# Kernel tuning notes

Hardware: AMD Instinct MI355X
Metric: run time of the kernel (lower is better)

Reference implementation:

```python
import jax, jax.numpy as jnp
import numpy as np
import math

SIZE = 11
PAD = 5
C1 = 0.01 ** 2
C2 = 0.03 ** 2


def gaussian_window():
    # Matches torch __init__: 1D gaussian (sigma=1.5), normalized, outer product,
    # expanded to depthwise weight of shape (3, 1, 11, 11)
    x = np.arange(SIZE, dtype=np.float32)
    g = np.exp(-((x - SIZE // 2) ** 2) / (2.0 * 1.5 ** 2)).astype(np.float32)
    g = g / g.sum()
    w2d = np.outer(g, g).astype(np.float32)  # (11, 11)
    return jnp.asarray(np.broadcast_to(w2d, (3, 1, SIZE, SIZE)).copy())


def depthwise_conv(x, win):
    return jax.lax.conv_general_dilated(
        x, win,
        window_strides=(1, 1),
        padding=[(PAD, PAD), (PAD, PAD)],
        dimension_numbers=('NCHW', 'OIHW', 'NCHW'),
        feature_group_count=3,
    )


def setup_inputs() -> dict:
    key = jax.random.key(0)
    k1, k2 = jax.random.split(key)
    img1 = jax.random.uniform(k1, (16, 3, 512, 512), dtype=jnp.float32)
    img2 = jax.random.uniform(k2, (16, 3, 512, 512), dtype=jnp.float32)
    return {"img1": img1, "img2": img2, "win": gaussian_window()}


def reference(img1, img2, win):
    mu1 = depthwise_conv(img1, win)
    mu2 = depthwise_conv(img2, win)
    mu1_sq = mu1 * mu1
    mu2_sq = mu2 * mu2
    mu1_mu2 = mu1 * mu2
    sig1_sq = depthwise_conv(img1 * img1, win) - mu1_sq
    sig2_sq = depthwise_conv(img2 * img2, win) - mu2_sq
    sig12 = depthwise_conv(img1 * img2, win) - mu1_mu2
    v = ((2.0 * mu1_mu2 + C1) * (2.0 * sig12 + C2)) / (
        (mu1_sq + mu2_sq + C1) * (sig1_sq + sig2_sq + C2))
    return 1.0 - jnp.mean(v)
```

## Files before the change

### kernel.cpp

```cpp
#include <hip/hip_runtime.h>


#define IMG 512
#define NPIX (16LL * 3 * 512 * 512)
#define GX 4
#define GY 16
#define NBLK (GX * GY * 48)
#define NPART (NBLK * 4)
#define HP 56

typedef short v8s __attribute__((ext_vector_type(8)));
typedef float v4f __attribute__((ext_vector_type(4)));
typedef __bf16 bf2 __attribute__((ext_vector_type(2)));
typedef float f2  __attribute__((ext_vector_type(2)));

static __device__ __forceinline__ int cvtpk2(f2 v) {
    bf2 r = __builtin_convertvector(v, bf2);
    return __builtin_bit_cast(int, r);
}
static __device__ __forceinline__ unsigned f2bf(float f) {
    unsigned u = __float_as_uint(f);
    return (u + 0x7FFFu + ((u >> 16) & 1u)) >> 16;
}

template <bool EDGE>
static __device__ __forceinline__ void load_tile(
    const float* __restrict__ p1, const float* __restrict__ p2,
    int ty0, int gct, int lm, int quad,
    float4 a[3][2], float4 b[3][2])
{
    const int gcol = gct * 16 - 8 + quad * 8;
    #pragma unroll
    for (int rt = 0; rt < 3; ++rt) {
        const int grow = ty0 - 8 + rt * 16 + lm;
        if (!EDGE) {
            const float* r1 = p1 + (size_t)grow * IMG + gcol;
            const float* r2 = p2 + (size_t)grow * IMG + gcol;
            a[rt][0] = *(const float4*)r1;  a[rt][1] = *(const float4*)(r1 + 4);
            b[rt][0] = *(const float4*)r2;  b[rt][1] = *(const float4*)(r2 + 4);
        } else {
            float4 z4; z4.x = z4.y = z4.z = z4.w = 0.f;
            a[rt][0] = a[rt][1] = b[rt][0] = b[rt][1] = z4;
            if ((unsigned)grow < IMG) {
                const float* r1 = p1 + (size_t)grow * IMG;
                const float* r2 = p2 + (size_t)grow * IMG;
                if ((unsigned)gcol < IMG) {
                    a[rt][0] = *(const float4*)(r1 + gcol);
                    b[rt][0] = *(const float4*)(r2 + gcol);
                }
                if ((unsigned)(gcol + 4) < IMG) {
                    a[rt][1] = *(const float4*)(r1 + gcol + 4);
                    b[rt][1] = *(const float4*)(r2 + gcol + 4);
                }
            }
        }
    }
}

static __device__ __forceinline__ void compute_tile(
    const float4 a[3][2], const float4 b[3][2], v8s band,
    short (*hw)[16][HP], int lm, int quad, f2& vsum)
{
    const v4f zacc = {0.f, 0.f, 0.f, 0.f};
    #pragma unroll
    for (int rt = 0; rt < 3; ++rt) {
        const float4 a0 = a[rt][0], a1 = a[rt][1];
        const float4 b0 = b[rt][0], b1 = b[rt][1];
        f2 a0l; a0l.x = a0.x; a0l.y = a0.y;   f2 a0h; a0h.x = a0.z; a0h.y = a0.w;
        f2 a1l; a1l.x = a1.x; a1l.y = a1.y;   f2 a1h; a1h.x = a1.z; a1h.y = a1.w;
        f2 b0l; b0l.x = b0.x; b0l.y = b0.y;   f2 b0h; b0h.x = b0.z; b0h.y = b0.w;
        f2 b1l; b1l.x = b1.x; b1l.y = b1.y;   f2 b1h; b1h.x = b1.z; b1h.y = b1.w;

        v8s A[4]; int4 w;
        w.x = cvtpk2(a0l); w.y = cvtpk2(a0h); w.z = cvtpk2(a1l); w.w = cvtpk2(a1h);
        A[0] = __builtin_bit_cast(v8s, w);
        w.x = cvtpk2(b0l); w.y = cvtpk2(b0h); w.z = cvtpk2(b1l); w.w = cvtpk2(b1h);
        A[1] = __builtin_bit_cast(v8s, w);
        w.x = cvtpk2(__builtin_elementwise_fma(a0l, a0l, b0l * b0l));
        w.y = cvtpk2(__builtin_elementwise_fma(a0h, a0h, b0h * b0h));
        w.z = cvtpk2(__builtin_elementwise_fma(a1l, a1l, b1l * b1l));
        w.w = cvtpk2(__builtin_elementwise_fma(a1h, a1h, b1h * b1h));
        A[2] = __builtin_bit_cast(v8s, w);
        w.x = cvtpk2(a0l * b0l); w.y = cvtpk2(a0h * b0h);
        w.z = cvtpk2(a1l * b1l); w.w = cvtpk2(a1h * b1h);
        A[3] = __builtin_bit_cast(v8s, w);

        #pragma unroll
        for (int p = 0; p < 4; ++p) {
            const v4f acc = __builtin_amdgcn_mfma_f32_16x16x32_bf16(A[p], band, zacc, 0, 0, 0);
            int2 w2;
            f2 lo; lo.x = acc[0]; lo.y = acc[1];
            f2 hi; hi.x = acc[2]; hi.y = acc[3];
            w2.x = cvtpk2(lo); w2.y = cvtpk2(hi);
            *(int2*)&hw[p][lm][rt * 16 + quad * 4] = w2;
        }
    }

    const f2 C1v = {1e-4f, 1e-4f};
    const f2 C2v = {9e-4f, 9e-4f};
    const f2 two = {2.f, 2.f};
    #pragma unroll
    for (int t2 = 0; t2 < 2; ++t2) {
        const int r0v = t2 * 16;
        v4f acc[4];
        #pragma unroll
        for (int p = 0; p < 4; ++p) {
            const v8s hf = *(const v8s*)&hw[p][lm][r0v + quad * 8];
            acc[p] = __builtin_amdgcn_mfma_f32_16x16x32_bf16(band, hf, zacc, 0, 0, 0);
        }
        #pragma unroll
        for (int h = 0; h < 2; ++h) {
            f2 m1; m1.x = acc[0][2 * h]; m1.y = acc[0][2 * h + 1];
            f2 m2; m2.x = acc[1][2 * h]; m2.y = acc[1][2 * h + 1];
            f2 es; es.x = acc[2][2 * h]; es.y = acc[2][2 * h + 1];
            f2 ex; ex.x = acc[3][2 * h]; ex.y = acc[3][2 * h + 1];
            const f2 m1s = m1 * m1, m2s = m2 * m2, m12 = m1 * m2;
            const f2 sig = es - m1s - m2s;
            const f2 s12 = ex - m12;
            const f2 num = __builtin_elementwise_fma(two, m12, C1v) *
                           __builtin_elementwise_fma(two, s12, C2v);
            const f2 den = (m1s + m2s + C1v) * (sig + C2v);
            f2 r; r.x = __builtin_amdgcn_rcpf(den.x); r.y = __builtin_amdgcn_rcpf(den.y);
            vsum = __builtin_elementwise_fma(num, r, vsum);
        }
    }
}

__global__ __launch_bounds__(256, 2) void ssim_kernel(
    const float* __restrict__ img1,
    const float* __restrict__ img2,
    const float* __restrict__ win,
    float* __restrict__ partial)
{
    __shared__ __align__(16) short hbuf[4][4][16][HP];

    const int tid  = threadIdx.x;
    const int lane = tid & 63;
    const int wave = tid >> 6;
    const int lm   = lane & 15;
    const int quad = lane >> 4;

    const int bx = blockIdx.x, by = blockIdx.y, z = blockIdx.z;
    const int ty0 = by * 32;

    float gl = 0.f;
    if (lane < 11) gl = win[55 + lane] * rsqrtf(win[60]);
    v8s band;
    #pragma unroll
    for (int j = 0; j < 8; ++j) {
        const int t  = quad * 8 + j - lm - 3;
        const int tc = ((unsigned)t > 10u) ? 11 : t;
        band[j] = (short)f2bf(__shfl(gl, tc));
    }

    const size_t zoff = (size_t)z * IMG * IMG;
    const float* p1 = img1 + zoff;
    const float* p2 = img2 + zoff;

    const int gct0 = bx * 8 + wave * 2;
    const int gct1 = gct0 + 1;
    const bool rowok = (by > 0) & (by < GY - 1);
    const bool int0  = rowok & (gct0 > 0) & (gct0 < 31);
    const bool int1  = rowok & (gct1 > 0) & (gct1 < 31);

    float4 a0[3][2], b0[3][2], a1[3][2], b1[3][2];
    if (int0) load_tile<false>(p1, p2, ty0, gct0, lm, quad, a0, b0);
    else      load_tile<true >(p1, p2, ty0, gct0, lm, quad, a0, b0);
    if (int1) load_tile<false>(p1, p2, ty0, gct1, lm, quad, a1, b1);
    else      load_tile<true >(p1, p2, ty0, gct1, lm, quad, a1, b1);

    f2 vsum = {0.f, 0.f};
    compute_tile(a0, b0, band, hbuf[wave], lm, quad, vsum);
    compute_tile(a1, b1, band, hbuf[wave], lm, quad, vsum);

    float vs = vsum.x + vsum.y;
    #pragma unroll
    for (int off = 32; off > 0; off >>= 1)
        vs += __shfl_down(vs, off, 64);
    if (lane == 0) {
        const int bidx = (z * (int)gridDim.y + by) * (int)gridDim.x + bx;
        partial[bidx * 4 + wave] = vs;
    }
}

__global__ __launch_bounds__(512) void finalize_kernel(
    const float* __restrict__ partial, float* __restrict__ out)
{
    __shared__ float red[8];
    const float4* p4 = (const float4*)partial;
    float s = 0.f;
    for (int i = threadIdx.x; i < NPART / 4; i += 512) {
        float4 t = p4[i];
        s += (t.x + t.y) + (t.z + t.w);
    }
    #pragma unroll
    for (int off = 32; off > 0; off >>= 1)
        s += __shfl_down(s, off, 64);
    if ((threadIdx.x & 63) == 0) red[threadIdx.x >> 6] = s;
    __syncthreads();
    if (threadIdx.x == 0) {
        float t = 0.f;
        #pragma unroll
        for (int i = 0; i < 8; ++i) t += red[i];
        out[0] = 1.0f - t / (float)NPIX;
    }
}

extern "C" void kernel_launch(void* const* d_in, const int* in_sizes, int n_in,
                              void* d_out, int out_size, void* d_ws, size_t ws_size,
                              hipStream_t stream) {
    const float* img1 = (const float*)d_in[0];
    const float* img2 = (const float*)d_in[1];
    const float* win  = (const float*)d_in[2];
    float* partialb = (float*)d_ws;

    dim3 grid(GX, GY, 48);
    ssim_kernel<<<grid, dim3(256), 0, stream>>>(img1, img2, win, partialb);
    finalize_kernel<<<1, dim3(512), 0, stream>>>(partialb, (float*)d_out);
}
```

Measured before the change: 143.0 us.

## Shrink per-wave work to one tile with ring-buffered LDS for higher occupancy

Each wave now processes one 16x16 output tile instead of two, so the grid doubles in x. The horizontal-pass buffer shrinks from 56 to 40 columns and is reused as a ring: the vertical pass for the first half runs before the third row-tile is written into slot 0. This lowers LDS and register use, letting launch bounds rise from 2 to 8 blocks per CU. Per-block partials are reduced through LDS into one value per block, and the finalize loop gets a fixed trip count and is unrolled. The cost is more blocks, less work per wave to hide latency, and an extra __syncthreads.

```diff
diff --git a/kernel.cpp b/kernel.cpp
--- a/kernel.cpp
+++ b/kernel.cpp
@@ -3,11 +3,10 @@
 
 #define IMG 512
 #define NPIX (16LL * 3 * 512 * 512)
-#define GX 4
+#define GX 8
 #define GY 16
 #define NBLK (GX * GY * 48)
-#define NPART (NBLK * 4)
-#define HP 56
+#define NPART NBLK
 
 typedef short v8s __attribute__((ext_vector_type(8)));
 typedef float v4f __attribute__((ext_vector_type(4)));
@@ -24,115 +23,107 @@
 }
 
 template <bool EDGE>
-static __device__ __forceinline__ void load_tile(
+static __device__ __forceinline__ void load_rt(
     const float* __restrict__ p1, const float* __restrict__ p2,
-    int ty0, int gct, int lm, int quad,
-    float4 a[3][2], float4 b[3][2])
-{
-    const int gcol = gct * 16 - 8 + quad * 8;
-    #pragma unroll
-    for (int rt = 0; rt < 3; ++rt) {
-        const int grow = ty0 - 8 + rt * 16 + lm;
-        if (!EDGE) {
-            const float* r1 = p1 + (size_t)grow * IMG + gcol;
-            const float* r2 = p2 + (size_t)grow * IMG + gcol;
-            a[rt][0] = *(const float4*)r1;  a[rt][1] = *(const float4*)(r1 + 4);
-            b[rt][0] = *(const float4*)r2;  b[rt][1] = *(const float4*)(r2 + 4);
-        } else {
-            float4 z4; z4.x = z4.y = z4.z = z4.w = 0.f;
-            a[rt][0] = a[rt][1] = b[rt][0] = b[rt][1] = z4;
-            if ((unsigned)grow < IMG) {
-                const float* r1 = p1 + (size_t)grow * IMG;
-                const float* r2 = p2 + (size_t)grow * IMG;
-                if ((unsigned)gcol < IMG) {
-                    a[rt][0] = *(const float4*)(r1 + gcol);
-                    b[rt][0] = *(const float4*)(r2 + gcol);
-                }
-                if ((unsigned)(gcol + 4) < IMG) {
-                    a[rt][1] = *(const float4*)(r1 + gcol + 4);
-                    b[rt][1] = *(const float4*)(r2 + gcol + 4);
-                }
+    int grow, int gcol,
+    float4& a0, float4& a1, float4& b0, float4& b1)
+{
+    if (!EDGE) {
+        const float* r1 = p1 + (size_t)grow * IMG + gcol;
+        const float* r2 = p2 + (size_t)grow * IMG + gcol;
+        a0 = *(const float4*)r1;       a1 = *(const float4*)(r1 + 4);
+        b0 = *(const float4*)r2;       b1 = *(const float4*)(r2 + 4);
+    } else {
+        float4 z4; z4.x = z4.y = z4.z = z4.w = 0.f;
+        a0 = a1 = b0 = b1 = z4;
+        if ((unsigned)grow < IMG) {
+            const float* r1 = p1 + (size_t)grow * IMG;
+            const float* r2 = p2 + (size_t)grow * IMG;
+            if ((unsigned)gcol < IMG) {
+                a0 = *(const float4*)(r1 + gcol);
+                b0 = *(const float4*)(r2 + gcol);
+            }
+            if ((unsigned)(gcol + 4) < IMG) {
+                a1 = *(const float4*)(r1 + gcol + 4);
+                b1 = *(const float4*)(r2 + gcol + 4);
             }
         }
     }
 }
 
-static __device__ __forceinline__ void compute_tile(
-    const float4 a[3][2], const float4 b[3][2], v8s band,
-    short (*hw)[16][HP], int lm, int quad, f2& vsum)
+static __device__ __forceinline__ void h_rt(
+    float4 a0, float4 a1, float4 b0, float4 b1,
+    v8s band, short (*hw)[16][40], int lm, int quad, int slot)
 {
     const v4f zacc = {0.f, 0.f, 0.f, 0.f};
-    #pragma unroll
-    for (int rt = 0; rt < 3; ++rt) {
-        const float4 a0 = a[rt][0], a1 = a[rt][1];
-        const float4 b0 = b[rt][0], b1 = b[rt][1];
-        f2 a0l; a0l.x = a0.x; a0l.y = a0.y;   f2 a0h; a0h.x = a0.z; a0h.y = a0.w;
-        f2 a1l; a1l.x = a1.x; a1l.y = a1.y;   f2 a1h; a1h.x = a1.z; a1h.y = a1.w;
-        f2 b0l; b0l.x = b0.x; b0l.y = b0.y;   f2 b0h; b0h.x = b0.z; b0h.y = b0.w;
-        f2 b1l; b1l.x = b1.x; b1l.y = b1.y;   f2 b1h; b1h.x = b1.z; b1h.y = b1.w;
-
-        v8s A[4]; int4 w;
-        w.x = cvtpk2(a0l); w.y = cvtpk2(a0h); w.z = cvtpk2(a1l); w.w = cvtpk2(a1h);
-        A[0] = __builtin_bit_cast(v8s, w);
-        w.x = cvtpk2(b0l); w.y = cvtpk2(b0h); w.z = cvtpk2(b1l); w.w = cvtpk2(b1h);
-        A[1] = __builtin_bit_cast(v8s, w);
-        w.x = cvtpk2(__builtin_elementwise_fma(a0l, a0l, b0l * b0l));
-        w.y = cvtpk2(__builtin_elementwise_fma(a0h, a0h, b0h * b0h));
-        w.z = cvtpk2(__builtin_elementwise_fma(a1l, a1l, b1l * b1l));
-        w.w = cvtpk2(__builtin_elementwise_fma(a1h, a1h, b1h * b1h));
-        A[2] = __builtin_bit_cast(v8s, w);
-        w.x = cvtpk2(a0l * b0l); w.y = cvtpk2(a0h * b0h);
-        w.z = cvtpk2(a1l * b1l); w.w = cvtpk2(a1h * b1h);
-        A[3] = __builtin_bit_cast(v8s, w);
-
-        #pragma unroll
-        for (int p = 0; p < 4; ++p) {
-            const v4f acc = __builtin_amdgcn_mfma_f32_16x16x32_bf16(A[p], band, zacc, 0, 0, 0);
-            int2 w2;
-            f2 lo; lo.x = acc[0]; lo.y = acc[1];
-            f2 hi; hi.x = acc[2]; hi.y = acc[3];
-            w2.x = cvtpk2(lo); w2.y = cvtpk2(hi);
-            *(int2*)&hw[p][lm][rt * 16 + quad * 4] = w2;
-        }
-    }
-
+    f2 a0l; a0l.x = a0.x; a0l.y = a0.y;   f2 a0h; a0h.x = a0.z; a0h.y = a0.w;
+    f2 a1l; a1l.x = a1.x; a1l.y = a1.y;   f2 a1h; a1h.x = a1.z; a1h.y = a1.w;
+    f2 b0l; b0l.x = b0.x; b0l.y = b0.y;   f2 b0h; b0h.x = b0.z; b0h.y = b0.w;
+    f2 b1l; b1l.x = b1.x; b1l.y = b1.y;   f2 b1h; b1h.x = b1.z; b1h.y = b1.w;
+
+    v8s A[4]; int4 w;
+    w.x = cvtpk2(a0l); w.y = cvtpk2(a0h); w.z = cvtpk2(a1l); w.w = cvtpk2(a1h);
+    A[0] = __builtin_bit_cast(v8s, w);
+    w.x = cvtpk2(b0l); w.y = cvtpk2(b0h); w.z = cvtpk2(b1l); w.w = cvtpk2(b1h);
+    A[1] = __builtin_bit_cast(v8s, w);
+    w.x = cvtpk2(__builtin_elementwise_fma(a0l, a0l, b0l * b0l));
+    w.y = cvtpk2(__builtin_elementwise_fma(a0h, a0h, b0h * b0h));
+    w.z = cvtpk2(__builtin_elementwise_fma(a1l, a1l, b1l * b1l));
+    w.w = cvtpk2(__builtin_elementwise_fma(a1h, a1h, b1h * b1h));
+    A[2] = __builtin_bit_cast(v8s, w);
+    w.x = cvtpk2(a0l * b0l); w.y = cvtpk2(a0h * b0h);
+    w.z = cvtpk2(a1l * b1l); w.w = cvtpk2(a1h * b1h);
+    A[3] = __builtin_bit_cast(v8s, w);
+
+    #pragma unroll
+    for (int p = 0; p < 4; ++p) {
+        const v4f acc = __builtin_amdgcn_mfma_f32_16x16x32_bf16(A[p], band, zacc, 0, 0, 0);
+        int2 w2;
+        f2 lo; lo.x = acc[0]; lo.y = acc[1];
+        f2 hi; hi.x = acc[2]; hi.y = acc[3];
+        w2.x = cvtpk2(lo); w2.y = cvtpk2(hi);
+        *(int2*)&hw[p][lm][slot * 16 + quad * 4] = w2;
+    }
+}
+
+static __device__ __forceinline__ void v_t2(
+    v8s band, short (*hw)[16][40], int lm, int quad, int t2, f2& vsum)
+{
+    const v4f zacc = {0.f, 0.f, 0.f, 0.f};
+    const int bs = (quad * 8 + t2 * 16) & 31;
+    v4f acc[4];
+    #pragma unroll
+    for (int p = 0; p < 4; ++p) {
+        const v8s hf = *(const v8s*)&hw[p][lm][bs];
+        acc[p] = __builtin_amdgcn_mfma_f32_16x16x32_bf16(band, hf, zacc, 0, 0, 0);
+    }
     const f2 C1v = {1e-4f, 1e-4f};
     const f2 C2v = {9e-4f, 9e-4f};
     const f2 two = {2.f, 2.f};
     #pragma unroll
-    for (int t2 = 0; t2 < 2; ++t2) {
-        const int r0v = t2 * 16;
-        v4f acc[4];
-        #pragma unroll
-        for (int p = 0; p < 4; ++p) {
-            const v8s hf = *(const v8s*)&hw[p][lm][r0v + quad * 8];
-            acc[p] = __builtin_amdgcn_mfma_f32_16x16x32_bf16(band, hf, zacc, 0, 0, 0);
-        }
-        #pragma unroll
-        for (int h = 0; h < 2; ++h) {
-            f2 m1; m1.x = acc[0][2 * h]; m1.y = acc[0][2 * h + 1];
-            f2 m2; m2.x = acc[1][2 * h]; m2.y = acc[1][2 * h + 1];
-            f2 es; es.x = acc[2][2 * h]; es.y = acc[2][2 * h + 1];
-            f2 ex; ex.x = acc[3][2 * h]; ex.y = acc[3][2 * h + 1];
-            const f2 m1s = m1 * m1, m2s = m2 * m2, m12 = m1 * m2;
-            const f2 sig = es - m1s - m2s;
-            const f2 s12 = ex - m12;
-            const f2 num = __builtin_elementwise_fma(two, m12, C1v) *
-                           __builtin_elementwise_fma(two, s12, C2v);
-            const f2 den = (m1s + m2s + C1v) * (sig + C2v);
-            f2 r; r.x = __builtin_amdgcn_rcpf(den.x); r.y = __builtin_amdgcn_rcpf(den.y);
-            vsum = __builtin_elementwise_fma(num, r, vsum);
-        }
-    }
-}
-
-__global__ __launch_bounds__(256, 2) void ssim_kernel(
+    for (int h = 0; h < 2; ++h) {
+        f2 m1; m1.x = acc[0][2 * h]; m1.y = acc[0][2 * h + 1];
+        f2 m2; m2.x = acc[1][2 * h]; m2.y = acc[1][2 * h + 1];
+        f2 es; es.x = acc[2][2 * h]; es.y = acc[2][2 * h + 1];
+        f2 ex; ex.x = acc[3][2 * h]; ex.y = acc[3][2 * h + 1];
+        const f2 m1s = m1 * m1, m2s = m2 * m2, m12 = m1 * m2;
+        const f2 sig = es - m1s - m2s;
+        const f2 s12 = ex - m12;
+        const f2 num = __builtin_elementwise_fma(two, m12, C1v) *
+                       __builtin_elementwise_fma(two, s12, C2v);
+        const f2 den = (m1s + m2s + C1v) * (sig + C2v);
+        f2 r; r.x = __builtin_amdgcn_rcpf(den.x); r.y = __builtin_amdgcn_rcpf(den.y);
+        vsum = __builtin_elementwise_fma(num, r, vsum);
+    }
+}
+
+__global__ __launch_bounds__(256, 8) void ssim_kernel(
     const float* __restrict__ img1,
     const float* __restrict__ img2,
     const float* __restrict__ win,
     float* __restrict__ partial)
 {
-    __shared__ __align__(16) short hbuf[4][4][16][HP];
+    __shared__ __align__(16) short hb[4][4][16][40];
 
     const int tid  = threadIdx.x;
     const int lane = tid & 63;
@@ -157,29 +148,42 @@
     const float* p1 = img1 + zoff;
     const float* p2 = img2 + zoff;
 
-    const int gct0 = bx * 8 + wave * 2;
-    const int gct1 = gct0 + 1;
-    const bool rowok = (by > 0) & (by < GY - 1);
-    const bool int0  = rowok & (gct0 > 0) & (gct0 < 31);
-    const bool int1  = rowok & (gct1 > 0) & (gct1 < 31);
-
-    float4 a0[3][2], b0[3][2], a1[3][2], b1[3][2];
-    if (int0) load_tile<false>(p1, p2, ty0, gct0, lm, quad, a0, b0);
-    else      load_tile<true >(p1, p2, ty0, gct0, lm, quad, a0, b0);
-    if (int1) load_tile<false>(p1, p2, ty0, gct1, lm, quad, a1, b1);
-    else      load_tile<true >(p1, p2, ty0, gct1, lm, quad, a1, b1);
+    const int gct = bx * 4 + wave;
+    const bool interior = (by > 0) & (by < GY - 1) & (gct > 0) & (gct < 31);
+    const int gcol = gct * 16 - 8 + quad * 8;
+    short (*hw)[16][40] = hb[wave];
+
+    float4 a[3][2], b[3][2];
+    if (interior) {
+        #pragma unroll
+        for (int rt = 0; rt < 3; ++rt)
+            load_rt<false>(p1, p2, ty0 - 8 + rt * 16 + lm, gcol,
+                           a[rt][0], a[rt][1], b[rt][0], b[rt][1]);
+    } else {
+        #pragma unroll
+        for (int rt = 0; rt < 3; ++rt)
+            load_rt<true >(p1, p2, ty0 - 8 + rt * 16 + lm, gcol,
+                           a[rt][0], a[rt][1], b[rt][0], b[rt][1]);
+    }
 
     f2 vsum = {0.f, 0.f};
-    compute_tile(a0, b0, band, hbuf[wave], lm, quad, vsum);
-    compute_tile(a1, b1, band, hbuf[wave], lm, quad, vsum);
+    h_rt(a[0][0], a[0][1], b[0][0], b[0][1], band, hw, lm, quad, 0);
+    h_rt(a[1][0], a[1][1], b[1][0], b[1][1], band, hw, lm, quad, 1);
+    v_t2(band, hw, lm, quad, 0, vsum);
+    h_rt(a[2][0], a[2][1], b[2][0], b[2][1], band, hw, lm, quad, 0);
+    v_t2(band, hw, lm, quad, 1, vsum);
 
     float vs = vsum.x + vsum.y;
     #pragma unroll
     for (int off = 32; off > 0; off >>= 1)
         vs += __shfl_down(vs, off, 64);
-    if (lane == 0) {
-        const int bidx = (z * (int)gridDim.y + by) * (int)gridDim.x + bx;
-        partial[bidx * 4 + wave] = vs;
+    if (lane == 0) *(float*)&hb[wave][3][15][36] = vs;
+    __syncthreads();
+    if (tid == 0) {
+        float t = 0.f;
+        #pragma unroll
+        for (int w = 0; w < 4; ++w) t += *(const float*)&hb[w][3][15][36];
+        partial[(z * GY + by) * GX + bx] = t;
     }
 }
 
@@ -189,8 +193,9 @@
     __shared__ float red[8];
     const float4* p4 = (const float4*)partial;
     float s = 0.f;
-    for (int i = threadIdx.x; i < NPART / 4; i += 512) {
-        float4 t = p4[i];
+    #pragma unroll
+    for (int i = 0; i < NPART / 4 / 512; ++i) {
+        const float4 t = p4[i * 512 + threadIdx.x];
         s += (t.x + t.y) + (t.z + t.w);
     }
     #pragma unroll
```

New measurement: 170.2 us. 1.19x slower.
